# Performance work log

Measured on AMD Instinct MI355X. Metric: run time of the kernel, lower is better.

The kernel has to match this reference:

```python
import jax, jax.numpy as jnp
import numpy as np

B, N, D, H = 4, 2048, 1024, 16
HD = D // H

def setup_inputs() -> dict:
    key = jax.random.key(0)
    ks = jax.random.split(key, 5)
    s = 0.02
    return {
        "x": jax.random.normal(ks[0], (B, N, D), dtype=jnp.float32),
        "W_qkv": jax.random.normal(ks[1], (D, 3 * D), dtype=jnp.float32) * s,
        "b_qkv": jnp.zeros((3 * D,), dtype=jnp.float32),
        "W_proj": jax.random.normal(ks[2], (D, D), dtype=jnp.float32) * s,
        "b_proj": jnp.zeros((D,), dtype=jnp.float32),
    }

def reference(x, W_qkv, b_qkv, W_proj, b_proj):
    scale = HD ** -0.5
    qkv = x @ W_qkv + b_qkv                       # [B,N,3D]
    qkv = qkv.reshape(B, N, 3, H, HD).transpose(2, 0, 3, 1, 4)  # [3,B,H,N,hd]
    q, k, v = qkv[0], qkv[1], qkv[2]
    attn = jnp.einsum('bhqd,bhkd->bhqk', q, k) * scale
    attn = jax.nn.softmax(attn, axis=-1)
    out = jnp.einsum('bhqk,bhkd->bhqd', attn, v)  # [B,H,N,hd]
    out = out.transpose(0, 2, 1, 3).reshape(B, N, D)
    return out @ W_proj + b_proj
```

## Files before the change

kernel.cpp:

```cpp
#include <hip/hip_runtime.h>


typedef __bf16 bf8v  __attribute__((ext_vector_type(8)));
typedef __bf16 bf4v  __attribute__((ext_vector_type(4)));
typedef float  f32x4 __attribute__((ext_vector_type(4)));

typedef const __attribute__((address_space(1))) void* gptr_t;
typedef __attribute__((address_space(3))) void*       lptr_t;

#define GLL16(g, l) __builtin_amdgcn_global_load_lds((gptr_t)(g), (lptr_t)(l), 16, 0, 0)

#define MFMA_BF16_16x16x32 __builtin_amdgcn_mfma_f32_16x16x32_bf16

static constexpr int Bsz = 4, Nseq = 2048, Dmod = 1024, H = 16, HD = 64;
static constexpr int Mtok = Bsz * Nseq;

__global__ __launch_bounds__(256) void cast_f32_bf16(const float* __restrict__ in,
                                                     __bf16* __restrict__ out, int n4) {
    int i = blockIdx.x * blockDim.x + threadIdx.x;
    int stride = gridDim.x * blockDim.x;
    for (; i < n4; i += stride) {
        float4 f = reinterpret_cast<const float4*>(in)[i];
        bf4v o;
        o[0] = (__bf16)f.x; o[1] = (__bf16)f.y; o[2] = (__bf16)f.z; o[3] = (__bf16)f.w;
        reinterpret_cast<bf4v*>(out)[i] = o;
    }
}

__global__ __launch_bounds__(256) void transpose_cast(const float* __restrict__ W,
                                                      __bf16* __restrict__ WT,
                                                      int K, int N) {
    __shared__ float t[32][33];
    int tx = threadIdx.x, ty = threadIdx.y;
    int bx = blockIdx.x, by = blockIdx.y;
#pragma unroll
    for (int j = 0; j < 4; ++j) {
        int k = by * 32 + ty + j * 8;
        int n = bx * 32 + tx;
        t[ty + j * 8][tx] = W[(size_t)k * N + n];
    }
    __syncthreads();
#pragma unroll
    for (int j = 0; j < 4; ++j) {
        int n = bx * 32 + ty + j * 8;
        int k = by * 32 + tx;
        WT[(size_t)n * K + k] = (__bf16)t[tx][ty + j * 8];
    }
}

template <int EPI>
__global__ __launch_bounds__(256) void gemm_bt(const __bf16* __restrict__ A,
                                               const __bf16* __restrict__ Bt,
                                               const float* __restrict__ bias,
                                               float* __restrict__ Cf,
                                               __bf16* __restrict__ Qo,
                                               __bf16* __restrict__ Ko,
                                               __bf16* __restrict__ Vo,
                                               int M, int N, int K) {
    __shared__ __attribute__((aligned(16))) __bf16 As[128 * 32];
    __shared__ __attribute__((aligned(16))) __bf16 Bs[128 * 32];

    const int nwg = gridDim.x;
    const int wg = (blockIdx.x & 7) * (nwg >> 3) + (blockIdx.x >> 3);

    const int nbn = N >> 7;
    const int bm = wg / nbn, bn = wg % nbn;
    const int tid = threadIdx.x;
    const int w = tid >> 6, l = tid & 63;
    const int wr = w >> 1, wc = w & 1;

    const int lr = l >> 2;
    const int lk = (l & 3) * 8;
    const int fr = l & 15;
    const int fk = (l >> 4) * 8;

    f32x4 acc[4][4] = {};

    for (int k0 = 0; k0 < K; k0 += 32) {
        const int c0 = w, c1 = w + 4;
        GLL16(A  + (size_t)(bm * 128 + c0 * 16 + lr) * K + k0 + lk, &As[c0 * 512]);
        GLL16(A  + (size_t)(bm * 128 + c1 * 16 + lr) * K + k0 + lk, &As[c1 * 512]);
        GLL16(Bt + (size_t)(bn * 128 + c0 * 16 + lr) * K + k0 + lk, &Bs[c0 * 512]);
        GLL16(Bt + (size_t)(bn * 128 + c1 * 16 + lr) * K + k0 + lk, &Bs[c1 * 512]);
        __syncthreads();

        bf8v af[4], bf[4];
#pragma unroll
        for (int m = 0; m < 4; ++m)
            af[m] = *(const bf8v*)&As[(wr * 64 + m * 16 + fr) * 32 + fk];
#pragma unroll
        for (int n = 0; n < 4; ++n)
            bf[n] = *(const bf8v*)&Bs[(wc * 64 + n * 16 + fr) * 32 + fk];
#pragma unroll
        for (int m = 0; m < 4; ++m)
#pragma unroll
            for (int n = 0; n < 4; ++n)
                acc[m][n] = MFMA_BF16_16x16x32(af[m], bf[n], acc[m][n], 0, 0, 0);
        __syncthreads();
    }

    const int r0 = bm * 128 + wr * 64;
    const int c0 = bn * 128 + wc * 64;
#pragma unroll
    for (int m = 0; m < 4; ++m)
#pragma unroll
        for (int n = 0; n < 4; ++n)
#pragma unroll
            for (int r = 0; r < 4; ++r) {
                int row = r0 + m * 16 + (l >> 4) * 4 + r;
                int col = c0 + n * 16 + (l & 15);
                float v = acc[m][n][r] + bias[col];
                if (EPI == 0) {
                    int mat = col >> 10, rem = col & 1023;
                    int h = rem >> 6, hd = rem & 63;
                    int b = row >> 11, nt = row & 2047;
                    __bf16 val = (__bf16)v;
                    if (mat == 0)
                        Qo[(((size_t)(b * H + h)) * Nseq + nt) * HD + hd] = val;
                    else if (mat == 1)
                        Ko[(((size_t)(b * H + h)) * Nseq + nt) * HD + hd] = val;
                    else
                        Vo[(((size_t)(b * H + h)) * HD + hd) * Nseq + nt] = val;
                } else {
                    Cf[(size_t)row * N + col] = v;
                }
            }
}

__global__ __launch_bounds__(256, 2) void attn_kernel(const __bf16* __restrict__ Q,
                                                      const __bf16* __restrict__ K,
                                                      const __bf16* __restrict__ VT,
                                                      __bf16* __restrict__ Ao) {
    __shared__ __attribute__((aligned(16))) __bf16 Ks[2][64 * 64];
    __shared__ __attribute__((aligned(16))) __bf16 Vts[2][64 * 64];
    __shared__ __attribute__((aligned(16))) __bf16 Pl[4][32 * 72];

    const int tid = threadIdx.x;
    const int w = tid >> 6, l = tid & 63;

    const int nwg = gridDim.x;
    const int id = (blockIdx.x & 7) * (nwg >> 3) + (blockIdx.x >> 3);
    const int qb = id & 15;
    const int h = (id >> 4) & 15;
    const int b = id >> 8;
    const size_t base = (size_t)(b * H + h) * Nseq * HD;

    const int fr = l & 15;
    const int fkh = (l >> 4) * 8;

    const int sr0 = tid >> 3, sp0 = tid & 7;
    const int sr1 = (256 + tid) >> 3, sp1 = tid & 7;

    bf8v qf[2][2];
#pragma unroll
    for (int m = 0; m < 2; ++m) {
        const int qrow = qb * 128 + w * 32 + m * 16 + fr;
        qf[m][0] = *(const bf8v*)&Q[base + (size_t)qrow * HD + fkh];
        qf[m][1] = *(const bf8v*)&Q[base + (size_t)qrow * HD + 32 + fkh];
#pragma unroll
        for (int j = 0; j < 8; ++j) {
            qf[m][0][j] = (__bf16)((float)qf[m][0][j] * 0.125f);
            qf[m][1][j] = (__bf16)((float)qf[m][1][j] * 0.125f);
        }
    }

    f32x4 o[2][4] = {};
    f32x4 psum[2] = {};

#define STAGE(buf, kt)                                                                   \
    do {                                                                                 \
        GLL16(K  + base + (size_t)((kt) * 64 + sr0) * HD + ((sp0 ^ (sr0 & 7)) << 3),     \
              &Ks[buf][(w * 64) * 8]);                                                   \
        GLL16(K  + base + (size_t)((kt) * 64 + sr1) * HD + ((sp1 ^ (sr1 & 7)) << 3),     \
              &Ks[buf][(256 + w * 64) * 8]);                                             \
        GLL16(VT + base + (size_t)sr0 * Nseq + (kt) * 64 + ((sp0 ^ (sr0 & 7)) << 3),     \
              &Vts[buf][(w * 64) * 8]);                                                  \
        GLL16(VT + base + (size_t)sr1 * Nseq + (kt) * 64 + ((sp1 ^ (sr1 & 7)) << 3),     \
              &Vts[buf][(256 + w * 64) * 8]);                                            \
    } while (0)

    STAGE(0, 0);

    for (int kt = 0; kt < Nseq / 64; ++kt) {
        const int cur = kt & 1;
        if (kt < Nseq / 64 - 1) {
            STAGE(cur ^ 1, kt + 1);
            asm volatile("s_waitcnt vmcnt(4)" ::: "memory");
        } else {
            asm volatile("s_waitcnt vmcnt(0)" ::: "memory");
        }
        __builtin_amdgcn_s_barrier();

        f32x4 s[2][4];
#pragma unroll
        for (int st = 0; st < 4; ++st) {
            const int krow = st * 16 + fr;
            const int key = (fr & 7) << 3;
            bf8v kf0 = *(const bf8v*)&Ks[cur][krow * 64 + (fkh ^ key)];
            bf8v kf1 = *(const bf8v*)&Ks[cur][krow * 64 + ((fkh + 32) ^ key)];
#pragma unroll
            for (int m = 0; m < 2; ++m) {
                f32x4 a = {};
                a = MFMA_BF16_16x16x32(qf[m][0], kf0, a, 0, 0, 0);
                a = MFMA_BF16_16x16x32(qf[m][1], kf1, a, 0, 0, 0);
                s[m][st] = a;
            }
        }

#pragma unroll
        for (int m = 0; m < 2; ++m)
#pragma unroll
            for (int st = 0; st < 4; ++st)
#pragma unroll
                for (int r = 0; r < 4; ++r) {
                    float p = __expf(s[m][st][r]);
                    psum[m][r] += p;
                    const int qr = m * 16 + (l >> 4) * 4 + r;
                    Pl[w][qr * 72 + st * 16 + (l & 15)] = (__bf16)p;
                }

        bf8v pa[2][2];
#pragma unroll
        for (int m = 0; m < 2; ++m) {
            const int prow = m * 16 + fr;
            pa[m][0] = *(const bf8v*)&Pl[w][prow * 72 + fkh];
            pa[m][1] = *(const bf8v*)&Pl[w][prow * 72 + 32 + fkh];
        }
#pragma unroll
        for (int t = 0; t < 4; ++t) {
            const int drow = t * 16 + fr;
            const int key = (fr & 7) << 3;
            bf8v vf0 = *(const bf8v*)&Vts[cur][drow * 64 + (fkh ^ key)];
            bf8v vf1 = *(const bf8v*)&Vts[cur][drow * 64 + ((fkh + 32) ^ key)];
#pragma unroll
            for (int m = 0; m < 2; ++m) {
                o[m][t] = MFMA_BF16_16x16x32(pa[m][0], vf0, o[m][t], 0, 0, 0);
                o[m][t] = MFMA_BF16_16x16x32(pa[m][1], vf1, o[m][t], 0, 0, 0);
            }
        }
        __builtin_amdgcn_s_barrier();
    }
#undef STAGE

#pragma unroll
    for (int m = 0; m < 2; ++m)
#pragma unroll
        for (int r = 0; r < 4; ++r) {
            float ps = psum[m][r];
#pragma unroll
            for (int off = 1; off < 16; off <<= 1) ps += __shfl_xor(ps, off);
            psum[m][r] = 1.f / ps;
        }
#pragma unroll
    for (int m = 0; m < 2; ++m)
#pragma unroll
        for (int t = 0; t < 4; ++t)
#pragma unroll
            for (int r = 0; r < 4; ++r) {
                const int row = m * 16 + (l >> 4) * 4 + r;
                const int nq = qb * 128 + w * 32 + row;
                const int hd = t * 16 + (l & 15);
                Ao[((size_t)(b * Nseq + nq)) * Dmod + h * HD + hd] =
                    (__bf16)(o[m][t][r] * psum[m][r]);
            }
}

extern "C" void kernel_launch(void* const* d_in, const int* in_sizes, int n_in,
                              void* d_out, int out_size, void* d_ws, size_t ws_size,
                              hipStream_t stream) {
    const float* x      = (const float*)d_in[0];
    const float* W_qkv  = (const float*)d_in[1];
    const float* b_qkv  = (const float*)d_in[2];
    const float* W_proj = (const float*)d_in[3];
    const float* b_proj = (const float*)d_in[4];
    float* out = (float*)d_out;

    char* ws = (char*)d_ws;
    __bf16* Xb     = (__bf16*)(ws);
    __bf16* WqkvT  = (__bf16*)(ws + 16777216);
    __bf16* WprojT = (__bf16*)(ws + 16777216 + 6291456);
    __bf16* Qb     = (__bf16*)(ws + 25165824);
    __bf16* Kb     = (__bf16*)(ws + 25165824 + 16777216);
    __bf16* VTb    = (__bf16*)(ws + 25165824 + 33554432);
    __bf16* Ab     = Xb;

    cast_f32_bf16<<<2048, 256, 0, stream>>>(x, Xb, Mtok * Dmod / 4);

    dim3 tb(32, 8);
    transpose_cast<<<dim3(3 * Dmod / 32, Dmod / 32), tb, 0, stream>>>(W_qkv, WqkvT, Dmod, 3 * Dmod);
    transpose_cast<<<dim3(Dmod / 32, Dmod / 32), tb, 0, stream>>>(W_proj, WprojT, Dmod, Dmod);

    gemm_bt<0><<<(Mtok / 128) * (3 * Dmod / 128), 256, 0, stream>>>(
        Xb, WqkvT, b_qkv, nullptr, Qb, Kb, VTb, Mtok, 3 * Dmod, Dmod);

    attn_kernel<<<Bsz * H * (Nseq / 128), 256, 0, stream>>>(Qb, Kb, VTb, Ab);

    gemm_bt<1><<<(Mtok / 128) * (Dmod / 128), 256, 0, stream>>>(
        Ab, WprojT, b_proj, out, nullptr, nullptr, nullptr, Mtok, Dmod, Dmod);
}
```

Before: 340.6 us.

## Widen GEMM K-tile with swizzled LDS, add separate V transpose, tune attention priority

The GEMM K step grows from 32 to 64, with an XOR-swizzled LDS layout meant to cut bank conflicts and halve the number of barriers per K. The QKV epilogue now writes V in row layout instead of the strided transposed scatter, and a new transpose_v kernel produces V^T through LDS. Workspace buffers are remapped so V^T reuses the X buffer. The attention kernel raises its occupancy hint to 3 and wraps its MFMA sections in s_setprio. The extra kernel adds launch overhead and a round trip of V through memory, and the swizzle index math in transpose_v looks fragile.

```diff
diff --git a/kernel.cpp b/kernel.cpp
--- a/kernel.cpp
+++ b/kernel.cpp
@@ -48,6 +48,35 @@
     }
 }
 
+__global__ __launch_bounds__(256) void transpose_v(const __bf16* __restrict__ V,
+                                                   __bf16* __restrict__ VT) {
+    __shared__ __bf16 Ls[64 * 72];
+    const int t = threadIdx.x;
+    const int blk = blockIdx.x;
+    const int nt0 = (blk & 31) * 64;
+    const size_t base = (size_t)(blk >> 5) * Nseq * HD;
+#pragma unroll
+    for (int i = 0; i < 2; ++i) {
+        int c = i * 256 + t;
+        int nt = c >> 3, p = c & 7;
+        bf8v v8 = *(const bf8v*)&V[base + (size_t)(nt0 + nt) * HD + p * 8];
+#pragma unroll
+        for (int j = 0; j < 8; ++j)
+            Ls[(p * 8 + j) * 72 + (nt ^ (p << 3))] = v8[j];
+    }
+    __syncthreads();
+#pragma unroll
+    for (int i = 0; i < 2; ++i) {
+        int c = i * 256 + t;
+        int hd = c >> 3, seg = c & 7;
+        int key = (hd >> 3) << 3;
+        bf8v o = *(const bf8v*)&Ls[hd * 72 + seg * 8];
+        int ntb = (seg * 8) ^ (key << 3);
+        ntb = (seg * 8) ^ ((hd >> 3) << 3);
+        *(bf8v*)&VT[base + (size_t)hd * Nseq + nt0 + ntb] = o;
+    }
+}
+
 template <int EPI>
 __global__ __launch_bounds__(256) void gemm_bt(const __bf16* __restrict__ A,
                                                const __bf16* __restrict__ Bt,
@@ -57,8 +86,8 @@
                                                __bf16* __restrict__ Ko,
                                                __bf16* __restrict__ Vo,
                                                int M, int N, int K) {
-    __shared__ __attribute__((aligned(16))) __bf16 As[128 * 32];
-    __shared__ __attribute__((aligned(16))) __bf16 Bs[128 * 32];
+    __shared__ __attribute__((aligned(16))) __bf16 As[128 * 64];
+    __shared__ __attribute__((aligned(16))) __bf16 Bs[128 * 64];
 
     const int nwg = gridDim.x;
     const int wg = (blockIdx.x & 7) * (nwg >> 3) + (blockIdx.x >> 3);
@@ -69,33 +98,47 @@
     const int w = tid >> 6, l = tid & 63;
     const int wr = w >> 1, wc = w & 1;
 
-    const int lr = l >> 2;
-    const int lk = (l & 3) * 8;
     const int fr = l & 15;
     const int fk = (l >> 4) * 8;
 
     f32x4 acc[4][4] = {};
 
-    for (int k0 = 0; k0 < K; k0 += 32) {
-        const int c0 = w, c1 = w + 4;
-        GLL16(A  + (size_t)(bm * 128 + c0 * 16 + lr) * K + k0 + lk, &As[c0 * 512]);
-        GLL16(A  + (size_t)(bm * 128 + c1 * 16 + lr) * K + k0 + lk, &As[c1 * 512]);
-        GLL16(Bt + (size_t)(bn * 128 + c0 * 16 + lr) * K + k0 + lk, &Bs[c0 * 512]);
-        GLL16(Bt + (size_t)(bn * 128 + c1 * 16 + lr) * K + k0 + lk, &Bs[c1 * 512]);
+    for (int k0 = 0; k0 < K; k0 += 64) {
+#pragma unroll
+        for (int i = 0; i < 4; ++i) {
+            int c = i * 256 + tid;
+            int row = c >> 3, col = (c & 7) * 8;
+            int scol = col ^ ((row & 7) << 3);
+            GLL16(A + (size_t)(bm * 128 + row) * K + k0 + scol, &As[(i * 256 + w * 64) * 8]);
+        }
+#pragma unroll
+        for (int i = 0; i < 4; ++i) {
+            int c = i * 256 + tid;
+            int row = c >> 3, col = (c & 7) * 8;
+            int scol = col ^ ((row & 7) << 3);
+            GLL16(Bt + (size_t)(bn * 128 + row) * K + k0 + scol, &Bs[(i * 256 + w * 64) * 8]);
+        }
         __syncthreads();
 
-        bf8v af[4], bf[4];
-#pragma unroll
-        for (int m = 0; m < 4; ++m)
-            af[m] = *(const bf8v*)&As[(wr * 64 + m * 16 + fr) * 32 + fk];
-#pragma unroll
-        for (int n = 0; n < 4; ++n)
-            bf[n] = *(const bf8v*)&Bs[(wc * 64 + n * 16 + fr) * 32 + fk];
-#pragma unroll
-        for (int m = 0; m < 4; ++m)
-#pragma unroll
-            for (int n = 0; n < 4; ++n)
-                acc[m][n] = MFMA_BF16_16x16x32(af[m], bf[n], acc[m][n], 0, 0, 0);
+#pragma unroll
+        for (int kk = 0; kk < 2; ++kk) {
+            bf8v af[4], bf[4];
+#pragma unroll
+            for (int m = 0; m < 4; ++m) {
+                int row = wr * 64 + m * 16 + fr;
+                af[m] = *(const bf8v*)&As[row * 64 + ((kk * 32 + fk) ^ ((row & 7) << 3))];
+            }
+#pragma unroll
+            for (int n = 0; n < 4; ++n) {
+                int row = wc * 64 + n * 16 + fr;
+                bf[n] = *(const bf8v*)&Bs[row * 64 + ((kk * 32 + fk) ^ ((row & 7) << 3))];
+            }
+#pragma unroll
+            for (int m = 0; m < 4; ++m)
+#pragma unroll
+                for (int n = 0; n < 4; ++n)
+                    acc[m][n] = MFMA_BF16_16x16x32(af[m], bf[n], acc[m][n], 0, 0, 0);
+        }
         __syncthreads();
     }
 
@@ -114,20 +157,18 @@
                     int mat = col >> 10, rem = col & 1023;
                     int h = rem >> 6, hd = rem & 63;
                     int b = row >> 11, nt = row & 2047;
+                    size_t dst = (((size_t)(b * H + h)) * Nseq + nt) * HD + hd;
                     __bf16 val = (__bf16)v;
-                    if (mat == 0)
-                        Qo[(((size_t)(b * H + h)) * Nseq + nt) * HD + hd] = val;
-                    else if (mat == 1)
-                        Ko[(((size_t)(b * H + h)) * Nseq + nt) * HD + hd] = val;
-                    else
-                        Vo[(((size_t)(b * H + h)) * HD + hd) * Nseq + nt] = val;
+                    if (mat == 0)      Qo[dst] = val;
+                    else if (mat == 1) Ko[dst] = val;
+                    else               Vo[dst] = val;
                 } else {
                     Cf[(size_t)row * N + col] = v;
                 }
             }
 }
 
-__global__ __launch_bounds__(256, 2) void attn_kernel(const __bf16* __restrict__ Q,
+__global__ __launch_bounds__(256, 3) void attn_kernel(const __bf16* __restrict__ Q,
                                                       const __bf16* __restrict__ K,
                                                       const __bf16* __restrict__ VT,
                                                       __bf16* __restrict__ Ao) {
@@ -192,6 +233,7 @@
         __builtin_amdgcn_s_barrier();
 
         f32x4 s[2][4];
+        __builtin_amdgcn_s_setprio(1);
 #pragma unroll
         for (int st = 0; st < 4; ++st) {
             const int krow = st * 16 + fr;
@@ -206,6 +248,7 @@
                 s[m][st] = a;
             }
         }
+        __builtin_amdgcn_s_setprio(0);
 
 #pragma unroll
         for (int m = 0; m < 2; ++m)
@@ -226,6 +269,7 @@
             pa[m][0] = *(const bf8v*)&Pl[w][prow * 72 + fkh];
             pa[m][1] = *(const bf8v*)&Pl[w][prow * 72 + 32 + fkh];
         }
+        __builtin_amdgcn_s_setprio(1);
 #pragma unroll
         for (int t = 0; t < 4; ++t) {
             const int drow = t * 16 + fr;
@@ -238,6 +282,7 @@
                 o[m][t] = MFMA_BF16_16x16x32(pa[m][1], vf1, o[m][t], 0, 0, 0);
             }
         }
+        __builtin_amdgcn_s_setprio(0);
         __builtin_amdgcn_s_barrier();
     }
 #undef STAGE
@@ -277,12 +322,13 @@
 
     char* ws = (char*)d_ws;
     __bf16* Xb     = (__bf16*)(ws);
+    __bf16* VTb    = (__bf16*)(ws);
     __bf16* WqkvT  = (__bf16*)(ws + 16777216);
-    __bf16* WprojT = (__bf16*)(ws + 16777216 + 6291456);
+    __bf16* WprojT = (__bf16*)(ws + 23068672);
     __bf16* Qb     = (__bf16*)(ws + 25165824);
-    __bf16* Kb     = (__bf16*)(ws + 25165824 + 16777216);
-    __bf16* VTb    = (__bf16*)(ws + 25165824 + 33554432);
-    __bf16* Ab     = Xb;
+    __bf16* Kb     = (__bf16*)(ws + 41943040);
+    __bf16* Vb     = (__bf16*)(ws + 58720256);
+    __bf16* Ab     = (__bf16*)(ws + 58720256);
 
     cast_f32_bf16<<<2048, 256, 0, stream>>>(x, Xb, Mtok * Dmod / 4);
 
@@ -291,7 +337,9 @@
     transpose_cast<<<dim3(Dmod / 32, Dmod / 32), tb, 0, stream>>>(W_proj, WprojT, Dmod, Dmod);
 
     gemm_bt<0><<<(Mtok / 128) * (3 * Dmod / 128), 256, 0, stream>>>(
-        Xb, WqkvT, b_qkv, nullptr, Qb, Kb, VTb, Mtok, 3 * Dmod, Dmod);
+        Xb, WqkvT, b_qkv, nullptr, Qb, Kb, Vb, Mtok, 3 * Dmod, Dmod);
+
+    transpose_v<<<Bsz * H * (Nseq / 64), 256, 0, stream>>>(Vb, VTb);
 
     attn_kernel<<<Bsz * H * (Nseq / 128), 256, 0, stream>>>(Qb, Kb, VTb, Ab);
 
```

Measured after the change: 299.8 us. -12.0%, faster.
